# Kernel optimization log

Hardware: AMD Instinct MI355X
Metric: run time of the kernel (lower is better)

The kernel has to match this reference:

```python
import jax, jax.numpy as jnp
import numpy as np

PAD = 1          # kernel offsets lie in [-1, 1] for kernel_size=3
COORD_MAX = 128  # coordinates quantized to [0, 128)
S = COORD_MAX + 2 * PAD  # per-dimension encoding stride (130)


def setup_inputs() -> dict:
    key = jax.random.key(0)
    B, N, D = 4, 50000, 3
    coordinates = jax.random.randint(
        jax.random.fold_in(key, 0), (B, N, D), 0, COORD_MAX, dtype=jnp.int32)
    # batch_indices[b, n] == b, matching how the torch code partitions rows
    batch_indices = jnp.broadcast_to(jnp.arange(B, dtype=jnp.int32)[:, None], (B, N))
    # 3^3 hypercube kernel offsets, lexicographic order (KernelGenerator semantics)
    r = jnp.arange(-1, 2, dtype=jnp.int32)
    kernel_offsets = jnp.stack(jnp.meshgrid(r, r, r, indexing='ij'), axis=-1).reshape(-1, 3)
    return {"coordinates": coordinates, "batch_indices": batch_indices,
            "kernel_offsets": kernel_offsets}


def reference(coordinates, batch_indices, kernel_offsets):
    """Vectorized equivalent of LocalSelfAttention.compute_kernel_mapping.

    Returns (input_idx, output_idx, rel_pos_idx, output_key_tensor, num_unique).
    The first three are [B, N, K] (the torch kernel_map flattened row-major is
    exactly zip of these), output_key_tensor is [L, D] padded with -1 beyond
    num_unique rows, with unique keys in first-occurrence (insertion) order --
    identical to the Python dict-hashing loop.
    """
    B, N, D = coordinates.shape
    K = kernel_offsets.shape[0]
    L = B * N * K

    # neighbor coords per (point, offset): [B, N, K, D]
    nb = coordinates[:, :, None, :] + kernel_offsets[None, None, :, :]

    # encode (batch_id, neighbor_coord) into a single int32 key
    enc = jnp.broadcast_to(batch_indices[:, :, None], (B, N, K)).astype(jnp.int32)
    for d in range(D):
        enc = enc * S + (nb[..., d] + PAD)  # max ~ 4*130^3 < 2^31
    keys = enc.reshape(L)

    # sort-based dedup preserving first-occurrence order
    order = jnp.argsort(keys, stable=True)              # [L]
    sk = keys[order]
    new_group = jnp.concatenate([jnp.ones((1,), bool), sk[1:] != sk[:-1]])
    gid_sorted = jnp.cumsum(new_group.astype(jnp.int32)) - 1  # group id per sorted slot
    num_unique = gid_sorted[-1] + 1

    # first flat position where each group's key occurs (empty groups -> int32 max)
    first_occ = jax.ops.segment_min(order, gid_sorted, num_segments=L)
    # insertion-order index of each group (padded groups stably rank last)
    group_rank = jnp.argsort(jnp.argsort(first_occ))

    # scatter group ids back to original flat order, then map to insertion rank
    gid = jnp.zeros((L,), jnp.int32).at[order].set(gid_sorted)
    output_idx = group_rank[gid].reshape(B, N, K).astype(jnp.int32)

    # representative encoded key per group, reordered to insertion order
    rep_key = jax.ops.segment_min(sk, gid_sorted, num_segments=L)
    enc_ord = jnp.zeros((L,), keys.dtype).at[group_rank].set(rep_key)

    # decode neighbor coordinates (drop the batch component, as torch does)
    coords_dec = []
    e = enc_ord
    for _ in range(D):
        coords_dec.append(e % S - PAD)
        e = e // S
    out_coords = jnp.stack(coords_dec[::-1], axis=-1)  # [L, D]
    valid = (jnp.arange(L) < num_unique)[:, None]
    output_key_tensor = jnp.where(valid, out_coords, -1)

    input_idx = jnp.broadcast_to(jnp.arange(N, dtype=jnp.int32)[None, :, None], (B, N, K))
    rel_pos_idx = jnp.broadcast_to(jnp.arange(K, dtype=jnp.int32)[None, None, :], (B, N, K))
    return (input_idx, output_idx, rel_pos_idx, output_key_tensor, num_unique)
```

## Files before the change

### kernel.cpp

```cpp
#include <hip/hip_runtime.h>
#include <cstdint>

#define B_   4
#define N_   50000
#define K_   27
#define P_   (B_ * N_)
#define L_   (P_ * K_)
#define S_   130
#define PL_  (S_ * S_)
#define KS_  (B_ * S_ * S_ * S_)
#define W_   (L_ / 64)
#define NBW  ((W_ + 255) / 256)
#define BIGP 0x7f7f7f7f

__global__ __launch_bounds__(256) void k_init(int4* __restrict__ T4) {
    const int n4 = KS_ / 4;
    int4 v = make_int4(BIGP, BIGP, BIGP, BIGP);
    for (int i = blockIdx.x * blockDim.x + threadIdx.x; i < n4; i += gridDim.x * blockDim.x)
        T4[i] = v;
}

__global__ __launch_bounds__(256) void k_ptab(const int* __restrict__ coords,
                                              const int* __restrict__ bidx,
                                              int* __restrict__ P1) {
    int p = blockIdx.x * blockDim.x + threadIdx.x;
    if (p >= P_) return;
    int b = bidx[p];
    int x = coords[3 * p + 0] + 1;
    int y = coords[3 * p + 1] + 1;
    int z = coords[3 * p + 2] + 1;
    int idx = ((b * S_ + x) * S_ + y) * S_ + z;
    atomicMin(&P1[idx], p << 5);
}

__global__ __launch_bounds__(256) void k_zy(const int* __restrict__ src,
                                            int* __restrict__ dst) {
    __shared__ int pl[PL_];
    __shared__ int tz[PL_];
    const int4* s4 = (const int4*)(src + (size_t)blockIdx.x * PL_);
    int4* d4       = (int4*)(dst + (size_t)blockIdx.x * PL_);
    int4* pl4      = (int4*)pl;
    for (int i = threadIdx.x; i < PL_ / 4; i += 256) pl4[i] = s4[i];
    __syncthreads();
    for (int i = threadIdx.x; i < PL_; i += 256) {
        int z = i % S_;
        int v = pl[i] + 1;
        if (z > 0)      v = min(v, pl[i - 1] + 2);
        if (z < S_ - 1) v = min(v, pl[i + 1]);
        tz[i] = v;
    }
    __syncthreads();
    for (int i = threadIdx.x; i < PL_ / 4; i += 256) {
        int4 o;
        int base = 4 * i;
        #pragma unroll
        for (int j = 0; j < 4; ++j) {
            int idx = base + j;
            int y = idx / S_;
            int v = tz[idx] + 3;
            if (y > 0)      v = min(v, tz[idx - S_] + 6);
            if (y < S_ - 1) v = min(v, tz[idx + S_]);
            ((int*)&o)[j] = v;
        }
        d4[i] = o;
    }
}

__global__ __launch_bounds__(256) void k_x(const int4* __restrict__ src,
                                           int4* __restrict__ dst) {
    const int n4 = KS_ / 4;
    int i = blockIdx.x * blockDim.x + threadIdx.x;
    if (i >= n4) return;
    int x = (i / (PL_ / 4)) % S_;
    int4 c = src[i];
    int4 v = make_int4(c.x + 9, c.y + 9, c.z + 9, c.w + 9);
    if (x > 0) {
        int4 m = src[i - PL_ / 4];
        v.x = min(v.x, m.x + 18); v.y = min(v.y, m.y + 18);
        v.z = min(v.z, m.z + 18); v.w = min(v.w, m.w + 18);
    }
    if (x < S_ - 1) {
        int4 pp = src[i + PL_ / 4];
        v.x = min(v.x, pp.x); v.y = min(v.y, pp.y);
        v.z = min(v.z, pp.z); v.w = min(v.w, pp.w);
    }
    dst[i] = v;
}

__global__ __launch_bounds__(256) void k_flag_bitmap(const int* __restrict__ coords,
                                                     const int* __restrict__ bidx,
                                                     const int* __restrict__ koffs,
                                                     const int* __restrict__ M,
                                                     int* __restrict__ mArr,
                                                     unsigned long long* __restrict__ bitmap,
                                                     int* __restrict__ out0,
                                                     int* __restrict__ out2) {
    int l = blockIdx.x * blockDim.x + threadIdx.x;
    if (l >= L_) return;
    int p = l / K_;
    int k = l - p * K_;
    out0[l] = p - (p / N_) * N_;
    out2[l] = k;
    int b = bidx[p];
    int cx = coords[3 * p + 0] + koffs[3 * k + 0] + 1;
    int cy = coords[3 * p + 1] + koffs[3 * k + 1] + 1;
    int cz = coords[3 * p + 2] + koffs[3 * k + 2] + 1;
    int idx = ((b * S_ + cx) * S_ + cy) * S_ + cz;
    int m32 = M[idx];
    mArr[l] = m32;
    unsigned long long bal = __ballot(m32 == ((p << 5) | k));
    if ((threadIdx.x & 63) == 0) bitmap[l >> 6] = bal;
}

__global__ __launch_bounds__(256) void k_scan_words(const unsigned long long* __restrict__ bitmap,
                                                    int* __restrict__ wpre,
                                                    int* __restrict__ bsum) {
    __shared__ int sh[256];
    int w = blockIdx.x * 256 + threadIdx.x;
    int c = (w < W_) ? __popcll(bitmap[w]) : 0;
    sh[threadIdx.x] = c;
    __syncthreads();
    for (int off = 1; off < 256; off <<= 1) {
        int t = (threadIdx.x >= off) ? sh[threadIdx.x - off] : 0;
        __syncthreads();
        sh[threadIdx.x] += t;
        __syncthreads();
    }
    if (w < W_) wpre[w] = sh[threadIdx.x] - c;
    if (threadIdx.x == 255) bsum[blockIdx.x] = sh[255];
}

__global__ __launch_bounds__(512) void k_scan_block(int* __restrict__ bsum,
                                                    int* __restrict__ num_unique_out) {
    __shared__ int sh[512];
    int i = threadIdx.x;
    int v = (i < NBW) ? bsum[i] : 0;
    sh[i] = v;
    __syncthreads();
    for (int off = 1; off < 512; off <<= 1) {
        int t = (i >= off) ? sh[i - off] : 0;
        __syncthreads();
        sh[i] += t;
        __syncthreads();
    }
    if (i < NBW) bsum[i] = sh[i] - v;
    if (i == 0) num_unique_out[0] = sh[511];
}

__global__ __launch_bounds__(256) void k_finalize(const int* __restrict__ coords,
                                                  const int* __restrict__ koffs,
                                                  const unsigned long long* __restrict__ bitmap,
                                                  const int* __restrict__ wpre,
                                                  const int* __restrict__ bsum,
                                                  const int* __restrict__ numuniq,
                                                  int* __restrict__ out1,
                                                  int* __restrict__ outkey) {
    int l = blockIdx.x * blockDim.x + threadIdx.x;
    if (l >= L_) return;
    int m32 = out1[l];
    int m = (m32 >> 5) * K_ + (m32 & 31);
    int w = m >> 6;
    unsigned long long word = bitmap[w];
    unsigned long long mask = (1ull << (m & 63)) - 1ull;
    int rank = wpre[w] + bsum[w >> 8] + (int)__popcll(word & mask);
    if (m == l) {
        int p = l / K_;
        int k = l - p * K_;
        outkey[3 * rank + 0] = coords[3 * p + 0] + koffs[3 * k + 0];
        outkey[3 * rank + 1] = coords[3 * p + 1] + koffs[3 * k + 1];
        outkey[3 * rank + 2] = coords[3 * p + 2] + koffs[3 * k + 2];
    }
    out1[l] = rank;
    if (l >= numuniq[0]) {
        outkey[3 * l + 0] = -1;
        outkey[3 * l + 1] = -1;
        outkey[3 * l + 2] = -1;
    }
}

extern "C" void kernel_launch(void* const* d_in, const int* in_sizes, int n_in,
                              void* d_out, int out_size, void* d_ws, size_t ws_size,
                              hipStream_t stream) {
    const int* coords = (const int*)d_in[0];
    const int* bidx   = (const int*)d_in[1];
    const int* koffs  = (const int*)d_in[2];

    int* out      = (int*)d_out;
    int* out0     = out;
    int* out1     = out + L_;
    int* out2     = out + 2 * L_;
    int* outkey   = out + 3 * L_;
    int* numuniq  = out + 6 * L_;

    int* P1 = (int*)d_ws;
    unsigned long long* bitmap = (unsigned long long*)(P1 + KS_);
    int* wpre = (int*)(bitmap + W_);
    int* bsum = wpre + W_;

    int* A = outkey;

    k_init        <<<2048, 256, 0, stream>>>((int4*)P1);
    k_ptab        <<<(P_ + 255) / 256, 256, 0, stream>>>(coords, bidx, P1);
    k_zy          <<<B_ * S_, 256, 0, stream>>>(P1, A);
    k_x           <<<(KS_ / 4 + 255) / 256, 256, 0, stream>>>((const int4*)A, (int4*)P1);
    k_flag_bitmap <<<(L_ + 255) / 256, 256, 0, stream>>>(coords, bidx, koffs, P1, out1, bitmap,
                                                         out0, out2);
    k_scan_words  <<<NBW, 256, 0, stream>>>(bitmap, wpre, bsum);
    k_scan_block  <<<1, 512, 0, stream>>>(bsum, numuniq);
    k_finalize    <<<(L_ + 255) / 256, 256, 0, stream>>>(coords, koffs, bitmap, wpre, bsum,
                                                         numuniq, out1, outkey);
}
```

Before: 174.6 us.

## Build first-occurrence bitmap from key table, fuse flag pass into finalize

Instead of a separate pass over all L entries that gathers the min-table value and ballots first-occurrence flags, the x-direction min pass now sets bits directly with atomicOr for every non-empty table cell, and the gather is folded into the finalize kernel. This removes one full L-sized kernel and the mArr write/read round trip, at the cost of zeroing the bitmap in init and issuing 64-bit atomics over the key table. The zy plane kernel also switches to 512-thread blocks. Atomic contention on bitmap words and the extra per-cell atomics over the 8.8M-entry table are the risk.

```diff
diff --git a/kernel.cpp b/kernel.cpp
--- a/kernel.cpp
+++ b/kernel.cpp
@@ -13,11 +13,14 @@
 #define NBW  ((W_ + 255) / 256)
 #define BIGP 0x7f7f7f7f
 
-__global__ __launch_bounds__(256) void k_init(int4* __restrict__ T4) {
+__global__ __launch_bounds__(256) void k_init(int4* __restrict__ T4,
+                                              unsigned long long* __restrict__ bitmap) {
     const int n4 = KS_ / 4;
     int4 v = make_int4(BIGP, BIGP, BIGP, BIGP);
     for (int i = blockIdx.x * blockDim.x + threadIdx.x; i < n4; i += gridDim.x * blockDim.x)
         T4[i] = v;
+    for (int i = blockIdx.x * blockDim.x + threadIdx.x; i < W_; i += gridDim.x * blockDim.x)
+        bitmap[i] = 0ull;
 }
 
 __global__ __launch_bounds__(256) void k_ptab(const int* __restrict__ coords,
@@ -33,16 +36,16 @@
     atomicMin(&P1[idx], p << 5);
 }
 
-__global__ __launch_bounds__(256) void k_zy(const int* __restrict__ src,
+__global__ __launch_bounds__(512) void k_zy(const int* __restrict__ src,
                                             int* __restrict__ dst) {
     __shared__ int pl[PL_];
     __shared__ int tz[PL_];
     const int4* s4 = (const int4*)(src + (size_t)blockIdx.x * PL_);
     int4* d4       = (int4*)(dst + (size_t)blockIdx.x * PL_);
     int4* pl4      = (int4*)pl;
-    for (int i = threadIdx.x; i < PL_ / 4; i += 256) pl4[i] = s4[i];
-    __syncthreads();
-    for (int i = threadIdx.x; i < PL_; i += 256) {
+    for (int i = threadIdx.x; i < PL_ / 4; i += 512) pl4[i] = s4[i];
+    __syncthreads();
+    for (int i = threadIdx.x; i < PL_; i += 512) {
         int z = i % S_;
         int v = pl[i] + 1;
         if (z > 0)      v = min(v, pl[i - 1] + 2);
@@ -50,7 +53,7 @@
         tz[i] = v;
     }
     __syncthreads();
-    for (int i = threadIdx.x; i < PL_ / 4; i += 256) {
+    for (int i = threadIdx.x; i < PL_ / 4; i += 512) {
         int4 o;
         int base = 4 * i;
         #pragma unroll
@@ -67,7 +70,8 @@
 }
 
 __global__ __launch_bounds__(256) void k_x(const int4* __restrict__ src,
-                                           int4* __restrict__ dst) {
+                                           int4* __restrict__ dst,
+                                           unsigned long long* __restrict__ bitmap) {
     const int n4 = KS_ / 4;
     int i = blockIdx.x * blockDim.x + threadIdx.x;
     if (i >= n4) return;
@@ -85,16 +89,63 @@
         v.z = min(v.z, pp.z); v.w = min(v.w, pp.w);
     }
     dst[i] = v;
-}
-
-__global__ __launch_bounds__(256) void k_flag_bitmap(const int* __restrict__ coords,
-                                                     const int* __restrict__ bidx,
-                                                     const int* __restrict__ koffs,
-                                                     const int* __restrict__ M,
-                                                     int* __restrict__ mArr,
-                                                     unsigned long long* __restrict__ bitmap,
-                                                     int* __restrict__ out0,
-                                                     int* __restrict__ out2) {
+    #pragma unroll
+    for (int j = 0; j < 4; ++j) {
+        int m32 = ((int*)&v)[j];
+        if (m32 < BIGP) {
+            int l = (m32 >> 5) * K_ + (m32 & 31);
+            atomicOr(&bitmap[l >> 6], 1ull << (l & 63));
+        }
+    }
+}
+
+__global__ __launch_bounds__(256) void k_scan_words(const unsigned long long* __restrict__ bitmap,
+                                                    int* __restrict__ wpre,
+                                                    int* __restrict__ bsum) {
+    __shared__ int sh[256];
+    int w = blockIdx.x * 256 + threadIdx.x;
+    int c = (w < W_) ? __popcll(bitmap[w]) : 0;
+    sh[threadIdx.x] = c;
+    __syncthreads();
+    for (int off = 1; off < 256; off <<= 1) {
+        int t = (threadIdx.x >= off) ? sh[threadIdx.x - off] : 0;
+        __syncthreads();
+        sh[threadIdx.x] += t;
+        __syncthreads();
+    }
+    if (w < W_) wpre[w] = sh[threadIdx.x] - c;
+    if (threadIdx.x == 255) bsum[blockIdx.x] = sh[255];
+}
+
+__global__ __launch_bounds__(512) void k_scan_block(int* __restrict__ bsum,
+                                                    int* __restrict__ num_unique_out) {
+    __shared__ int sh[512];
+    int i = threadIdx.x;
+    int v = (i < NBW) ? bsum[i] : 0;
+    sh[i] = v;
+    __syncthreads();
+    for (int off = 1; off < 512; off <<= 1) {
+        int t = (i >= off) ? sh[i - off] : 0;
+        __syncthreads();
+        sh[i] += t;
+        __syncthreads();
+    }
+    if (i < NBW) bsum[i] = sh[i] - v;
+    if (i == 0) num_unique_out[0] = sh[511];
+}
+
+__global__ __launch_bounds__(256) void k_finalize(const int* __restrict__ coords,
+                                                  const int* __restrict__ bidx,
+                                                  const int* __restrict__ koffs,
+                                                  const int* __restrict__ M,
+                                                  const unsigned long long* __restrict__ bitmap,
+                                                  const int* __restrict__ wpre,
+                                                  const int* __restrict__ bsum,
+                                                  const int* __restrict__ numuniq,
+                                                  int* __restrict__ out0,
+                                                  int* __restrict__ out1,
+                                                  int* __restrict__ out2,
+                                                  int* __restrict__ outkey) {
     int l = blockIdx.x * blockDim.x + threadIdx.x;
     if (l >= L_) return;
     int p = l / K_;
@@ -107,70 +158,17 @@
     int cz = coords[3 * p + 2] + koffs[3 * k + 2] + 1;
     int idx = ((b * S_ + cx) * S_ + cy) * S_ + cz;
     int m32 = M[idx];
-    mArr[l] = m32;
-    unsigned long long bal = __ballot(m32 == ((p << 5) | k));
-    if ((threadIdx.x & 63) == 0) bitmap[l >> 6] = bal;
-}
-
-__global__ __launch_bounds__(256) void k_scan_words(const unsigned long long* __restrict__ bitmap,
-                                                    int* __restrict__ wpre,
-                                                    int* __restrict__ bsum) {
-    __shared__ int sh[256];
-    int w = blockIdx.x * 256 + threadIdx.x;
-    int c = (w < W_) ? __popcll(bitmap[w]) : 0;
-    sh[threadIdx.x] = c;
-    __syncthreads();
-    for (int off = 1; off < 256; off <<= 1) {
-        int t = (threadIdx.x >= off) ? sh[threadIdx.x - off] : 0;
-        __syncthreads();
-        sh[threadIdx.x] += t;
-        __syncthreads();
-    }
-    if (w < W_) wpre[w] = sh[threadIdx.x] - c;
-    if (threadIdx.x == 255) bsum[blockIdx.x] = sh[255];
-}
-
-__global__ __launch_bounds__(512) void k_scan_block(int* __restrict__ bsum,
-                                                    int* __restrict__ num_unique_out) {
-    __shared__ int sh[512];
-    int i = threadIdx.x;
-    int v = (i < NBW) ? bsum[i] : 0;
-    sh[i] = v;
-    __syncthreads();
-    for (int off = 1; off < 512; off <<= 1) {
-        int t = (i >= off) ? sh[i - off] : 0;
-        __syncthreads();
-        sh[i] += t;
-        __syncthreads();
-    }
-    if (i < NBW) bsum[i] = sh[i] - v;
-    if (i == 0) num_unique_out[0] = sh[511];
-}
-
-__global__ __launch_bounds__(256) void k_finalize(const int* __restrict__ coords,
-                                                  const int* __restrict__ koffs,
-                                                  const unsigned long long* __restrict__ bitmap,
-                                                  const int* __restrict__ wpre,
-                                                  const int* __restrict__ bsum,
-                                                  const int* __restrict__ numuniq,
-                                                  int* __restrict__ out1,
-                                                  int* __restrict__ outkey) {
-    int l = blockIdx.x * blockDim.x + threadIdx.x;
-    if (l >= L_) return;
-    int m32 = out1[l];
     int m = (m32 >> 5) * K_ + (m32 & 31);
     int w = m >> 6;
     unsigned long long word = bitmap[w];
     unsigned long long mask = (1ull << (m & 63)) - 1ull;
     int rank = wpre[w] + bsum[w >> 8] + (int)__popcll(word & mask);
+    out1[l] = rank;
     if (m == l) {
-        int p = l / K_;
-        int k = l - p * K_;
-        outkey[3 * rank + 0] = coords[3 * p + 0] + koffs[3 * k + 0];
-        outkey[3 * rank + 1] = coords[3 * p + 1] + koffs[3 * k + 1];
-        outkey[3 * rank + 2] = coords[3 * p + 2] + koffs[3 * k + 2];
-    }
-    out1[l] = rank;
+        outkey[3 * rank + 0] = cx - 1;
+        outkey[3 * rank + 1] = cy - 1;
+        outkey[3 * rank + 2] = cz - 1;
+    }
     if (l >= numuniq[0]) {
         outkey[3 * l + 0] = -1;
         outkey[3 * l + 1] = -1;
@@ -199,14 +197,13 @@
 
     int* A = outkey;
 
-    k_init        <<<2048, 256, 0, stream>>>((int4*)P1);
-    k_ptab        <<<(P_ + 255) / 256, 256, 0, stream>>>(coords, bidx, P1);
-    k_zy          <<<B_ * S_, 256, 0, stream>>>(P1, A);
-    k_x           <<<(KS_ / 4 + 255) / 256, 256, 0, stream>>>((const int4*)A, (int4*)P1);
-    k_flag_bitmap <<<(L_ + 255) / 256, 256, 0, stream>>>(coords, bidx, koffs, P1, out1, bitmap,
-                                                         out0, out2);
-    k_scan_words  <<<NBW, 256, 0, stream>>>(bitmap, wpre, bsum);
-    k_scan_block  <<<1, 512, 0, stream>>>(bsum, numuniq);
-    k_finalize    <<<(L_ + 255) / 256, 256, 0, stream>>>(coords, koffs, bitmap, wpre, bsum,
-                                                         numuniq, out1, outkey);
-}
+    k_init       <<<2048, 256, 0, stream>>>((int4*)P1, bitmap);
+    k_ptab       <<<(P_ + 255) / 256, 256, 0, stream>>>(coords, bidx, P1);
+    k_zy         <<<B_ * S_, 512, 0, stream>>>(P1, A);
+    k_x          <<<(KS_ / 4 + 255) / 256, 256, 0, stream>>>((const int4*)A, (int4*)P1, bitmap);
+    k_scan_words <<<NBW, 256, 0, stream>>>(bitmap, wpre, bsum);
+    k_scan_block <<<1, 512, 0, stream>>>(bsum, numuniq);
+    k_finalize   <<<(L_ + 255) / 256, 256, 0, stream>>>(coords, bidx, koffs, P1,
+                                                        bitmap, wpre, bsum, numuniq,
+                                                        out0, out1, out2, outkey);
+}
```

Result: slower. 295.3 us (+69.1%).
